# Kernel optimization log

Hardware: AMD Instinct MI355X
Metric: run time of the kernel (lower is better)

Reference implementation:

```python
import jax, jax.numpy as jnp
import numpy as np

E, H, KV, D = 2048, 32, 8, 64  # embed_dim, n_head, n_kv_head, head_dim
B, C = 1, 2048
G = H // KV  # GQA group size = 4


def setup_inputs() -> dict:
    key = jax.random.key(0)
    k0, k1, k2, k3, k4 = jax.random.split(key, 5)
    s = 0.02
    return {
        "x": jax.random.normal(k0, (B, C, E), dtype=jnp.float32),
        "W_q": jax.random.normal(k1, (H * D, E), dtype=jnp.float32) * s,
        "W_k": jax.random.normal(k2, (KV * D, E), dtype=jnp.float32) * s,
        "W_v": jax.random.normal(k3, (KV * D, E), dtype=jnp.float32) * s,
        "W_o": jax.random.normal(k4, (E, H * D), dtype=jnp.float32) * s,
    }


def reference(x, W_q, W_k, W_v, W_o):
    b, c, e = x.shape
    # bias-free projections (nn.Linear applies x @ W.T)
    Q = (x @ W_q.T).reshape(b, c, KV, G, D)   # [B,C,KV,G,D]
    K = (x @ W_k.T).reshape(b, c, KV, D)      # [B,C,KV,D]
    V = (x @ W_v.T).reshape(b, c, KV, D)
    scale = 1.0 / jnp.sqrt(jnp.float32(D))
    # grouped-query attention scores: query heads grouped per KV head
    scores = jnp.einsum("bqkgd,bskd->bkgqs", Q, K) * scale  # [B,KV,G,Cq,Cs]
    causal = jnp.tril(jnp.ones((c, c), dtype=bool))
    scores = jnp.where(causal, scores, jnp.finfo(scores.dtype).min)
    attn = jax.nn.softmax(scores, axis=-1)
    hidden = jnp.einsum("bkgqs,bskd->bqkgd", attn, V)  # [B,Cq,KV,G,D]
    hidden = hidden.reshape(b, c, H * D)
    return hidden @ W_o.T
```

## Files before the change

kernel.cpp:

```cpp
#include <hip/hip_runtime.h>
#include <stdint.h>
#include <stddef.h>

#define CLEN 2048
#define EMB  2048
#define NH   32
#define NKV  8
#define HD   64

#define SZ_X  (CLEN * EMB)
#define SZ_WQ (NH * HD * EMB)
#define SZ_WK (NKV * HD * EMB)
#define SZ_WV (NKV * HD * EMB)
#define SZ_WO (EMB * NH * HD)
#define SZ_ALL (SZ_X + SZ_WQ + SZ_WK + SZ_WV + SZ_WO)

typedef __attribute__((ext_vector_type(8))) short short8v;
typedef __attribute__((ext_vector_type(4))) short short4v;
typedef __attribute__((ext_vector_type(4))) float float4v;

#define MFMA16(A, B, C) __builtin_amdgcn_mfma_f32_16x16x32_bf16((A), (B), (C), 0, 0, 0)

#define SCL 0.1803368801111244f

__device__ __forceinline__ uint16_t f2bf(float f) {
  union { float f; unsigned int u; } c;
  c.f = f;
  return (uint16_t)((c.u + 0x7fffu + ((c.u >> 16) & 1u)) >> 16);
}
__device__ __forceinline__ uint16_t f2bf_c(float f) {
  union { float f; unsigned int u; } c;
  c.f = f;
  return (uint16_t)((c.u + 0x8000u) >> 16);
}

__device__ __forceinline__ void gload_lds16(const uint16_t* g, uint16_t* l) {
  __builtin_amdgcn_global_load_lds((const __attribute__((address_space(1))) void*)g,
                                   (__attribute__((address_space(3))) void*)l, 16, 0, 0);
}

__global__ __launch_bounds__(256) void cvt_all(
    const float* __restrict__ s0, const float* __restrict__ s1,
    const float* __restrict__ s2, const float* __restrict__ s3,
    const float* __restrict__ s4, uint16_t* __restrict__ dst)
{
  const long i = ((long)blockIdx.x * 256 + threadIdx.x) * 4;
  if (i >= SZ_ALL) return;
  const float* src;
  long off;
  if (i < SZ_X)                         { src = s0; off = i; }
  else if (i < SZ_X + SZ_WQ)            { src = s1; off = i - SZ_X; }
  else if (i < SZ_X + SZ_WQ + SZ_WK)    { src = s2; off = i - (SZ_X + SZ_WQ); }
  else if (i < SZ_X + SZ_WQ + SZ_WK + SZ_WV) { src = s3; off = i - (SZ_X + SZ_WQ + SZ_WK); }
  else                                  { src = s4; off = i - (SZ_X + SZ_WQ + SZ_WK + SZ_WV); }
  const float4v v = *(const float4v*)(src + off);
  short4v p;
#pragma unroll
  for (int j = 0; j < 4; ++j) p[j] = (short)f2bf(v[j]);
  *(short4v*)(dst + i) = p;
}

template <int NW, int OMODE>
__device__ __forceinline__ void gemm_bk64(
    const uint16_t* __restrict__ A, const uint16_t* __restrict__ B,
    uint16_t* __restrict__ Co, float* __restrict__ Cf,
    int m0, int n0, int M, int N, int Kd, float oscale)
{
  __shared__ uint16_t As[128 * 64];
  __shared__ uint16_t Bs[32 * NW * 64];
  const int tid = threadIdx.x;
  const int w = tid >> 6, l = tid & 63;
  const int wr = (w >> 1) << 5;
  const int wc = (w & 1) * (NW << 4);
  const int lr = l & 15, lhi = l >> 4;
  const int swz = (lr & 7) << 4;

  float4v acc[2][NW] = {};

  const int sr8 = l >> 3;
  const int scol = (((l & 7) ^ sr8) << 3);

  for (int k0 = 0; k0 < Kd; k0 += 64) {
    __syncthreads();
    gload_lds16(A + (size_t)(m0 + (w << 3) + sr8) * Kd + k0 + scol,       As + w * 512);
    gload_lds16(A + (size_t)(m0 + ((w + 8) << 3) + sr8) * Kd + k0 + scol, As + (w + 8) * 512);
    gload_lds16(B + (size_t)(n0 + (w << 3) + sr8) * Kd + k0 + scol,       Bs + w * 512);
    if (NW == 4)
      gload_lds16(B + (size_t)(n0 + ((w + 8) << 3) + sr8) * Kd + k0 + scol, Bs + (w + 8) * 512);
    __syncthreads();

    short8v a[2][2], b[NW][2];
#pragma unroll
    for (int i = 0; i < 2; ++i) {
      const int row = wr + i * 16 + lr;
#pragma unroll
      for (int ks = 0; ks < 2; ++ks)
        a[i][ks] = *(const short8v*)((const char*)As + row * 128 + ((ks * 64 + lhi * 16) ^ swz));
    }
#pragma unroll
    for (int j = 0; j < NW; ++j) {
      const int row = wc + j * 16 + lr;
#pragma unroll
      for (int ks = 0; ks < 2; ++ks)
        b[j][ks] = *(const short8v*)((const char*)Bs + row * 128 + ((ks * 64 + lhi * 16) ^ swz));
    }
#pragma unroll
    for (int ks = 0; ks < 2; ++ks)
#pragma unroll
      for (int i = 0; i < 2; ++i)
#pragma unroll
        for (int j = 0; j < NW; ++j)
          acc[i][j] = MFMA16(a[i][ks], b[j][ks], acc[i][j]);
  }

  if (OMODE == 1) {
#pragma unroll
    for (int i = 0; i < 2; ++i) {
      const int m = m0 + wr + i * 16 + lhi * 4;
#pragma unroll
      for (int j = 0; j < NW; ++j) {
        const int n = n0 + wc + j * 16 + lr;
        short4v pk;
#pragma unroll
        for (int r = 0; r < 4; ++r) pk[r] = (short)f2bf(acc[i][j][r]);
        *(short4v*)(Co + (size_t)n * M + m) = pk;
      }
    }
  } else if (OMODE == 0) {
#pragma unroll
    for (int i = 0; i < 2; ++i) {
      const int m = m0 + wr + i * 16 + lhi * 4;
#pragma unroll
      for (int j = 0; j < NW; ++j) {
        const int n = n0 + wc + j * 16 + lr;
#pragma unroll
        for (int r = 0; r < 4; ++r)
          Co[(size_t)(m + r) * N + n] = f2bf(acc[i][j][r] * oscale);
      }
    }
  } else {
#pragma unroll
    for (int i = 0; i < 2; ++i) {
      const int m = m0 + wr + i * 16 + lhi * 4;
#pragma unroll
      for (int j = 0; j < NW; ++j) {
        const int n = n0 + wc + j * 16 + lr;
#pragma unroll
        for (int r = 0; r < 4; ++r)
          Cf[(size_t)(m + r) * N + n] = acc[i][j][r];
      }
    }
  }
}

__global__ __launch_bounds__(512) void qkv_gemm(
    const uint16_t* __restrict__ x,
    const uint16_t* __restrict__ Wq, const uint16_t* __restrict__ Wk,
    const uint16_t* __restrict__ Wv,
    uint16_t* __restrict__ Qw, uint16_t* __restrict__ Kw, uint16_t* __restrict__ Vtw)
{
  const int m0 = blockIdx.x << 7;
  const int bn = blockIdx.y;
  if (bn < 16) {
    gemm_bk64<4, 0>(x, Wq, Qw, nullptr, m0, bn << 7, CLEN, NH * HD, EMB, SCL);
  } else if (bn < 24) {
    gemm_bk64<2, 0>(x, Wk, Kw, nullptr, m0, (bn - 16) << 6, CLEN, NKV * HD, EMB, 1.0f);
  } else {
    gemm_bk64<2, 1>(x, Wv, Vtw, nullptr, m0, (bn - 24) << 6, CLEN, NKV * HD, EMB, 1.0f);
  }
}

__global__ __launch_bounds__(512) void out_gemm(
    const uint16_t* __restrict__ Hh, const uint16_t* __restrict__ Wo,
    float* __restrict__ out)
{
  gemm_bk64<2, 2>(Hh, Wo, nullptr, out, blockIdx.x << 7, blockIdx.y << 6, CLEN, EMB, NH * HD, 1.0f);
}

__global__ __launch_bounds__(512) void attn_fwd(
    const uint16_t* __restrict__ Q, const uint16_t* __restrict__ Kx,
    const uint16_t* __restrict__ Vt, uint16_t* __restrict__ Hd)
{
  const int kvh = blockIdx.y;
  const int xp = blockIdx.x;
  const int tid = threadIdx.x, w = tid >> 6, l = tid & 63;
  const int lr = l & 15, lhi = l >> 4;
  const int h = (kvh << 2) | (w >> 1);
  const int wq = (w & 1) << 4;

  __shared__ uint16_t Ks[2][64 * 64];
  __shared__ uint16_t Vs[2][64 * 64];
  __shared__ uint16_t Pl[8][16 * 72];

  short8v ones;
#pragma unroll
  for (int c = 0; c < 8; ++c) ones[c] = (short)0x3F80;

  const int sr8 = l >> 3;
  const int scol = (((l & 7) ^ sr8) << 3);
  const int srow = (w << 3) | sr8;

  for (int it = 0; it < 2; ++it) {
    const int x = it ? (63 - xp) : xp;
    const int q0 = x << 5;
    const int qoff = (x & 1) << 5;
    const int ntile = (x >> 1) + 1;

    short8v qf0, qf1;
    {
      const uint16_t* qp = Q + (size_t)(q0 + wq + lr) * (NH * HD) + h * HD + lhi * 8;
      qf0 = *(const short8v*)qp;
      qf1 = *(const short8v*)(qp + 32);
    }

    float4v o[4] = {};
    float4v osum = {};

    gload_lds16(Kx + (size_t)srow * (NKV * HD) + kvh * HD + scol, Ks[0] + w * 512);
    gload_lds16(Vt + (size_t)(kvh * HD + srow) * CLEN + scol,     Vs[0] + w * 512);
    __syncthreads();

    int cur = 0;
    for (int s = 0; s < ntile; ++s) {
      if (s + 1 < ntile) {
        const int kv1 = (s + 1) << 6;
        gload_lds16(Kx + (size_t)(kv1 + srow) * (NKV * HD) + kvh * HD + scol,
                    Ks[cur ^ 1] + w * 512);
        gload_lds16(Vt + (size_t)(kvh * HD + srow) * CLEN + kv1 + scol,
                    Vs[cur ^ 1] + w * 512);
      }

      const char* KsB = (const char*)Ks[cur];
      const char* VsB = (const char*)Vs[cur];

      float4v sf[4];
      __builtin_amdgcn_s_setprio(1);
#pragma unroll
      for (int nb = 0; nb < 4; ++nb) {
        const int row = nb * 16 + lr;
        const int rowb = row * 128, sw = (row & 7) << 4;
        float4v a0 = {};
        a0 = MFMA16(qf0, *(const short8v*)(KsB + ((rowb + lhi * 16) ^ sw)), a0);
        a0 = MFMA16(qf1, *(const short8v*)(KsB + ((rowb + 64 + lhi * 16) ^ sw)), a0);
        sf[nb] = a0;
      }
      __builtin_amdgcn_s_setprio(0);

      if (s == ntile - 1) {
        const int qb = qoff + wq + lhi * 4;
#pragma unroll
        for (int nb = 0; nb < 4; ++nb)
#pragma unroll
          for (int r = 0; r < 4; ++r) {
            const float vv = (nb * 16 + lr <= qb + r) ? sf[nb][r] : -3e38f;
            sf[nb][r] = __builtin_amdgcn_exp2f(vv);
          }
      } else {
#pragma unroll
        for (int nb = 0; nb < 4; ++nb)
#pragma unroll
          for (int r = 0; r < 4; ++r)
            sf[nb][r] = __builtin_amdgcn_exp2f(sf[nb][r]);
      }

#pragma unroll
      for (int nb = 0; nb < 4; ++nb)
#pragma unroll
        for (int r = 0; r < 4; ++r)
          Pl[w][(lhi * 4 + r) * 72 + nb * 16 + lr] = f2bf_c(sf[nb][r]);
      const short8v pf0 = *(const short8v*)&Pl[w][lr * 72 + lhi * 8];
      const short8v pf1 = *(const short8v*)&Pl[w][lr * 72 + 32 + lhi * 8];

      __builtin_amdgcn_s_setprio(1);
#pragma unroll
      for (int j = 0; j < 4; ++j) {
        const int row = j * 16 + lr;
        const int rowb = row * 128, sw = (row & 7) << 4;
        o[j] = MFMA16(pf0, *(const short8v*)(VsB + ((rowb + lhi * 16) ^ sw)), o[j]);
        o[j] = MFMA16(pf1, *(const short8v*)(VsB + ((rowb + 64 + lhi * 16) ^ sw)), o[j]);
      }
      osum = MFMA16(pf0, ones, osum);
      osum = MFMA16(pf1, ones, osum);
      __builtin_amdgcn_s_setprio(0);

      __syncthreads();
      cur ^= 1;
    }

#pragma unroll
    for (int r = 0; r < 4; ++r) {
      const float inv = 1.0f / osum[r];
      const size_t qq = (size_t)(q0 + wq + lhi * 4 + r);
#pragma unroll
      for (int j = 0; j < 4; ++j)
        Hd[qq * (NH * HD) + h * HD + j * 16 + lr] = f2bf(o[j][r] * inv);
    }
  }
}

extern "C" void kernel_launch(void* const* d_in, const int* in_sizes, int n_in,
                              void* d_out, int out_size, void* d_ws, size_t ws_size,
                              hipStream_t stream) {
  const float* x  = (const float*)d_in[0];
  const float* Wq = (const float*)d_in[1];
  const float* Wk = (const float*)d_in[2];
  const float* Wv = (const float*)d_in[3];
  const float* Wo = (const float*)d_in[4];

  uint16_t* ws  = (uint16_t*)d_ws;
  uint16_t* xb  = ws;
  uint16_t* Wqb = xb  + SZ_X;
  uint16_t* Wkb = Wqb + SZ_WQ;
  uint16_t* Wvb = Wkb + SZ_WK;
  uint16_t* Wob = Wvb + SZ_WV;
  uint16_t* Qw  = Wob + SZ_WO;
  uint16_t* Kw  = Qw  + (size_t)CLEN * (NH * HD);
  uint16_t* Vtw = Kw  + (size_t)CLEN * (NKV * HD);
  uint16_t* Hw  = Vtw + (size_t)CLEN * (NKV * HD);

  cvt_all<<<SZ_ALL / 1024, 256, 0, stream>>>(x, Wq, Wk, Wv, Wo, ws);
  qkv_gemm<<<dim3(16, 32), 512, 0, stream>>>(xb, Wqb, Wkb, Wvb, Qw, Kw, Vtw);
  attn_fwd<<<dim3(32, 8), 512, 0, stream>>>(Qw, Kw, Vtw, Hw);
  out_gemm<<<dim3(16, 32), 512, 0, stream>>>(Hw, Wob, (float*)d_out);
}
```

Before: 114.9 us.

## Software-pipeline attention loop: overlap PV of previous tile with QK of current

```diff
diff --git a/kernel.cpp b/kernel.cpp
--- a/kernel.cpp
+++ b/kernel.cpp
@@ -189,7 +189,7 @@
   const int wq = (w & 1) << 4;
 
   __shared__ uint16_t Ks[2][64 * 64];
-  __shared__ uint16_t Vs[2][64 * 64];
+  __shared__ uint16_t Vs[3][64 * 64];
   __shared__ uint16_t Pl[8][16 * 72];
 
   short8v ones;
@@ -215,76 +215,87 @@
 
     float4v o[4] = {};
     float4v osum = {};
+    short8v pfP0 = {}, pfP1 = {};
 
     gload_lds16(Kx + (size_t)srow * (NKV * HD) + kvh * HD + scol, Ks[0] + w * 512);
     gload_lds16(Vt + (size_t)(kvh * HD + srow) * CLEN + scol,     Vs[0] + w * 512);
     __syncthreads();
 
-    int cur = 0;
-    for (int s = 0; s < ntile; ++s) {
-      if (s + 1 < ntile) {
-        const int kv1 = (s + 1) << 6;
+    int vw = 1;
+    int vr = 0;
+
+    for (int i = 0; i <= ntile; ++i) {
+      if (i + 1 < ntile) {
+        const int kv1 = (i + 1) << 6;
         gload_lds16(Kx + (size_t)(kv1 + srow) * (NKV * HD) + kvh * HD + scol,
-                    Ks[cur ^ 1] + w * 512);
+                    Ks[(i + 1) & 1] + w * 512);
         gload_lds16(Vt + (size_t)(kvh * HD + srow) * CLEN + kv1 + scol,
-                    Vs[cur ^ 1] + w * 512);
-      }
-
-      const char* KsB = (const char*)Ks[cur];
-      const char* VsB = (const char*)Vs[cur];
-
-      float4v sf[4];
-      __builtin_amdgcn_s_setprio(1);
-#pragma unroll
-      for (int nb = 0; nb < 4; ++nb) {
-        const int row = nb * 16 + lr;
-        const int rowb = row * 128, sw = (row & 7) << 4;
-        float4v a0 = {};
-        a0 = MFMA16(qf0, *(const short8v*)(KsB + ((rowb + lhi * 16) ^ sw)), a0);
-        a0 = MFMA16(qf1, *(const short8v*)(KsB + ((rowb + 64 + lhi * 16) ^ sw)), a0);
-        sf[nb] = a0;
-      }
-      __builtin_amdgcn_s_setprio(0);
-
-      if (s == ntile - 1) {
-        const int qb = qoff + wq + lhi * 4;
+                    Vs[vw] + w * 512);
+        vw = (vw == 2) ? 0 : vw + 1;
+      }
+
+      short8v pfC0, pfC1;
+      bool haveC = (i < ntile);
+      if (haveC) {
+        const char* KsB = (const char*)Ks[i & 1];
+        float4v sf[4];
+        __builtin_amdgcn_s_setprio(1);
+#pragma unroll
+        for (int nb = 0; nb < 4; ++nb) {
+          const int row = nb * 16 + lr;
+          const int rowb = row * 128, sw = (row & 7) << 4;
+          float4v a0 = {};
+          a0 = MFMA16(qf0, *(const short8v*)(KsB + ((rowb + lhi * 16) ^ sw)), a0);
+          a0 = MFMA16(qf1, *(const short8v*)(KsB + ((rowb + 64 + lhi * 16) ^ sw)), a0);
+          sf[nb] = a0;
+        }
+        __builtin_amdgcn_s_setprio(0);
+
+        if (i == ntile - 1) {
+          const int qb = qoff + wq + lhi * 4;
+#pragma unroll
+          for (int nb = 0; nb < 4; ++nb)
+#pragma unroll
+            for (int r = 0; r < 4; ++r) {
+              const float vv = (nb * 16 + lr <= qb + r) ? sf[nb][r] : -3e38f;
+              sf[nb][r] = __builtin_amdgcn_exp2f(vv);
+            }
+        } else {
+#pragma unroll
+          for (int nb = 0; nb < 4; ++nb)
+#pragma unroll
+            for (int r = 0; r < 4; ++r)
+              sf[nb][r] = __builtin_amdgcn_exp2f(sf[nb][r]);
+        }
+
 #pragma unroll
         for (int nb = 0; nb < 4; ++nb)
 #pragma unroll
-          for (int r = 0; r < 4; ++r) {
-            const float vv = (nb * 16 + lr <= qb + r) ? sf[nb][r] : -3e38f;
-            sf[nb][r] = __builtin_amdgcn_exp2f(vv);
-          }
-      } else {
-#pragma unroll
-        for (int nb = 0; nb < 4; ++nb)
-#pragma unroll
           for (int r = 0; r < 4; ++r)
-            sf[nb][r] = __builtin_amdgcn_exp2f(sf[nb][r]);
-      }
-
-#pragma unroll
-      for (int nb = 0; nb < 4; ++nb)
-#pragma unroll
-        for (int r = 0; r < 4; ++r)
-          Pl[w][(lhi * 4 + r) * 72 + nb * 16 + lr] = f2bf_c(sf[nb][r]);
-      const short8v pf0 = *(const short8v*)&Pl[w][lr * 72 + lhi * 8];
-      const short8v pf1 = *(const short8v*)&Pl[w][lr * 72 + 32 + lhi * 8];
-
-      __builtin_amdgcn_s_setprio(1);
-#pragma unroll
-      for (int j = 0; j < 4; ++j) {
-        const int row = j * 16 + lr;
-        const int rowb = row * 128, sw = (row & 7) << 4;
-        o[j] = MFMA16(pf0, *(const short8v*)(VsB + ((rowb + lhi * 16) ^ sw)), o[j]);
-        o[j] = MFMA16(pf1, *(const short8v*)(VsB + ((rowb + 64 + lhi * 16) ^ sw)), o[j]);
-      }
-      osum = MFMA16(pf0, ones, osum);
-      osum = MFMA16(pf1, ones, osum);
-      __builtin_amdgcn_s_setprio(0);
+            Pl[w][(lhi * 4 + r) * 72 + nb * 16 + lr] = f2bf_c(sf[nb][r]);
+        pfC0 = *(const short8v*)&Pl[w][lr * 72 + lhi * 8];
+        pfC1 = *(const short8v*)&Pl[w][lr * 72 + 32 + lhi * 8];
+      }
+
+      if (i >= 1) {
+        const char* VsB = (const char*)Vs[vr];
+        vr = (vr == 2) ? 0 : vr + 1;
+        __builtin_amdgcn_s_setprio(1);
+#pragma unroll
+        for (int j = 0; j < 4; ++j) {
+          const int row = j * 16 + lr;
+          const int rowb = row * 128, sw = (row & 7) << 4;
+          o[j] = MFMA16(pfP0, *(const short8v*)(VsB + ((rowb + lhi * 16) ^ sw)), o[j]);
+          o[j] = MFMA16(pfP1, *(const short8v*)(VsB + ((rowb + 64 + lhi * 16) ^ sw)), o[j]);
+        }
+        osum = MFMA16(pfP0, ones, osum);
+        osum = MFMA16(pfP1, ones, osum);
+        __builtin_amdgcn_s_setprio(0);
+      }
+
+      if (haveC) { pfP0 = pfC0; pfP1 = pfC1; }
 
       __syncthreads();
-      cur ^= 1;
     }
 
 #pragma unroll
```

After: 121.1 us. 1.05x slower.

## Halve attention block to 4 waves, each covering 32 query rows

Applied to the files above, without the earlier changes.

```diff
diff --git a/kernel.cpp b/kernel.cpp
--- a/kernel.cpp
+++ b/kernel.cpp
@@ -177,7 +177,7 @@
   gemm_bk64<2, 2>(Hh, Wo, nullptr, out, blockIdx.x << 7, blockIdx.y << 6, CLEN, EMB, NH * HD, 1.0f);
 }
 
-__global__ __launch_bounds__(512) void attn_fwd(
+__global__ __launch_bounds__(256) void attn_fwd(
     const uint16_t* __restrict__ Q, const uint16_t* __restrict__ Kx,
     const uint16_t* __restrict__ Vt, uint16_t* __restrict__ Hd)
 {
@@ -185,12 +185,12 @@
   const int xp = blockIdx.x;
   const int tid = threadIdx.x, w = tid >> 6, l = tid & 63;
   const int lr = l & 15, lhi = l >> 4;
-  const int h = (kvh << 2) | (w >> 1);
-  const int wq = (w & 1) << 4;
+  const int h = (kvh << 2) | w;
+  const int swz = (lr & 7) << 4;
 
   __shared__ uint16_t Ks[2][64 * 64];
   __shared__ uint16_t Vs[2][64 * 64];
-  __shared__ uint16_t Pl[8][16 * 72];
+  __shared__ uint16_t Pl[4][32 * 72];
 
   short8v ones;
 #pragma unroll
@@ -198,7 +198,6 @@
 
   const int sr8 = l >> 3;
   const int scol = (((l & 7) ^ sr8) << 3);
-  const int srow = (w << 3) | sr8;
 
   for (int it = 0; it < 2; ++it) {
     const int x = it ? (63 - xp) : xp;
@@ -206,81 +205,122 @@
     const int qoff = (x & 1) << 5;
     const int ntile = (x >> 1) + 1;
 
-    short8v qf0, qf1;
-    {
-      const uint16_t* qp = Q + (size_t)(q0 + wq + lr) * (NH * HD) + h * HD + lhi * 8;
-      qf0 = *(const short8v*)qp;
-      qf1 = *(const short8v*)(qp + 32);
-    }
-
-    float4v o[4] = {};
-    float4v osum = {};
-
-    gload_lds16(Kx + (size_t)srow * (NKV * HD) + kvh * HD + scol, Ks[0] + w * 512);
-    gload_lds16(Vt + (size_t)(kvh * HD + srow) * CLEN + scol,     Vs[0] + w * 512);
+    short8v qf[2][2];
+#pragma unroll
+    for (int i = 0; i < 2; ++i) {
+      const uint16_t* qp = Q + (size_t)(q0 + i * 16 + lr) * (NH * HD) + h * HD + lhi * 8;
+      qf[i][0] = *(const short8v*)qp;
+      qf[i][1] = *(const short8v*)(qp + 32);
+    }
+
+    float4v o[2][4] = {};
+    float4v osum[2] = {};
+
+#pragma unroll
+    for (int ci = 0; ci < 2; ++ci) {
+      const int c = (ci << 2) | w;
+      const int srow = (c << 3) | sr8;
+      gload_lds16(Kx + (size_t)srow * (NKV * HD) + kvh * HD + scol, Ks[0] + c * 512);
+      gload_lds16(Vt + (size_t)(kvh * HD + srow) * CLEN + scol,     Vs[0] + c * 512);
+    }
     __syncthreads();
 
     int cur = 0;
     for (int s = 0; s < ntile; ++s) {
       if (s + 1 < ntile) {
         const int kv1 = (s + 1) << 6;
-        gload_lds16(Kx + (size_t)(kv1 + srow) * (NKV * HD) + kvh * HD + scol,
-                    Ks[cur ^ 1] + w * 512);
-        gload_lds16(Vt + (size_t)(kvh * HD + srow) * CLEN + kv1 + scol,
-                    Vs[cur ^ 1] + w * 512);
+#pragma unroll
+        for (int ci = 0; ci < 2; ++ci) {
+          const int c = (ci << 2) | w;
+          const int srow = (c << 3) | sr8;
+          gload_lds16(Kx + (size_t)(kv1 + srow) * (NKV * HD) + kvh * HD + scol,
+                      Ks[cur ^ 1] + c * 512);
+          gload_lds16(Vt + (size_t)(kvh * HD + srow) * CLEN + kv1 + scol,
+                      Vs[cur ^ 1] + c * 512);
+        }
       }
 
       const char* KsB = (const char*)Ks[cur];
       const char* VsB = (const char*)Vs[cur];
 
-      float4v sf[4];
+      short8v kb[4][2];
+#pragma unroll
+      for (int nb = 0; nb < 4; ++nb) {
+        const int rowb = (nb * 16 + lr) * 128;
+#pragma unroll
+        for (int ks = 0; ks < 2; ++ks)
+          kb[nb][ks] = *(const short8v*)(KsB + ((rowb) + ((ks * 64 + lhi * 16) ^ swz)));
+      }
+
+      float4v sf[2][4];
       __builtin_amdgcn_s_setprio(1);
 #pragma unroll
-      for (int nb = 0; nb < 4; ++nb) {
-        const int row = nb * 16 + lr;
-        const int rowb = row * 128, sw = (row & 7) << 4;
-        float4v a0 = {};
-        a0 = MFMA16(qf0, *(const short8v*)(KsB + ((rowb + lhi * 16) ^ sw)), a0);
-        a0 = MFMA16(qf1, *(const short8v*)(KsB + ((rowb + 64 + lhi * 16) ^ sw)), a0);
-        sf[nb] = a0;
-      }
+      for (int i = 0; i < 2; ++i)
+#pragma unroll
+        for (int nb = 0; nb < 4; ++nb) {
+          float4v a0 = {};
+          a0 = MFMA16(qf[i][0], kb[nb][0], a0);
+          a0 = MFMA16(qf[i][1], kb[nb][1], a0);
+          sf[i][nb] = a0;
+        }
       __builtin_amdgcn_s_setprio(0);
 
       if (s == ntile - 1) {
-        const int qb = qoff + wq + lhi * 4;
+#pragma unroll
+        for (int i = 0; i < 2; ++i) {
+          const int qb = qoff + i * 16 + lhi * 4;
+#pragma unroll
+          for (int nb = 0; nb < 4; ++nb)
+#pragma unroll
+            for (int r = 0; r < 4; ++r) {
+              const float vv = (nb * 16 + lr <= qb + r) ? sf[i][nb][r] : -3e38f;
+              sf[i][nb][r] = __builtin_amdgcn_exp2f(vv);
+            }
+        }
+      } else {
+#pragma unroll
+        for (int i = 0; i < 2; ++i)
+#pragma unroll
+          for (int nb = 0; nb < 4; ++nb)
+#pragma unroll
+            for (int r = 0; r < 4; ++r)
+              sf[i][nb][r] = __builtin_amdgcn_exp2f(sf[i][nb][r]);
+      }
+
+#pragma unroll
+      for (int i = 0; i < 2; ++i)
 #pragma unroll
         for (int nb = 0; nb < 4; ++nb)
 #pragma unroll
-          for (int r = 0; r < 4; ++r) {
-            const float vv = (nb * 16 + lr <= qb + r) ? sf[nb][r] : -3e38f;
-            sf[nb][r] = __builtin_amdgcn_exp2f(vv);
-          }
-      } else {
-#pragma unroll
-        for (int nb = 0; nb < 4; ++nb)
-#pragma unroll
           for (int r = 0; r < 4; ++r)
-            sf[nb][r] = __builtin_amdgcn_exp2f(sf[nb][r]);
-      }
-
-#pragma unroll
-      for (int nb = 0; nb < 4; ++nb)
-#pragma unroll
-        for (int r = 0; r < 4; ++r)
-          Pl[w][(lhi * 4 + r) * 72 + nb * 16 + lr] = f2bf_c(sf[nb][r]);
-      const short8v pf0 = *(const short8v*)&Pl[w][lr * 72 + lhi * 8];
-      const short8v pf1 = *(const short8v*)&Pl[w][lr * 72 + 32 + lhi * 8];
+            Pl[w][(i * 16 + lhi * 4 + r) * 72 + nb * 16 + lr] = f2bf_c(sf[i][nb][r]);
+      short8v pf[2][2];
+#pragma unroll
+      for (int i = 0; i < 2; ++i)
+#pragma unroll
+        for (int ks = 0; ks < 2; ++ks)
+          pf[i][ks] = *(const short8v*)&Pl[w][(i * 16 + lr) * 72 + ks * 32 + lhi * 8];
+
+      short8v vb[4][2];
+#pragma unroll
+      for (int j = 0; j < 4; ++j) {
+        const int rowb = (j * 16 + lr) * 128;
+#pragma unroll
+        for (int ks = 0; ks < 2; ++ks)
+          vb[j][ks] = *(const short8v*)(VsB + ((rowb) + ((ks * 64 + lhi * 16) ^ swz)));
+      }
 
       __builtin_amdgcn_s_setprio(1);
 #pragma unroll
-      for (int j = 0; j < 4; ++j) {
-        const int row = j * 16 + lr;
-        const int rowb = row * 128, sw = (row & 7) << 4;
-        o[j] = MFMA16(pf0, *(const short8v*)(VsB + ((rowb + lhi * 16) ^ sw)), o[j]);
-        o[j] = MFMA16(pf1, *(const short8v*)(VsB + ((rowb + 64 + lhi * 16) ^ sw)), o[j]);
-      }
-      osum = MFMA16(pf0, ones, osum);
-      osum = MFMA16(pf1, ones, osum);
+      for (int i = 0; i < 2; ++i) {
+#pragma unroll
+        for (int j = 0; j < 4; ++j) {
+          o[i][j] = MFMA16(pf[i][0], vb[j][0], o[i][j]);
+          o[i][j] = MFMA16(pf[i][1], vb[j][1], o[i][j]);
+        }
+        osum[i] = MFMA16(pf[i][0], ones, osum[i]);
+        osum[i] = MFMA16(pf[i][1], ones, osum[i]);
+      }
       __builtin_amdgcn_s_setprio(0);
 
       __syncthreads();
@@ -288,13 +328,15 @@
     }
 
 #pragma unroll
-    for (int r = 0; r < 4; ++r) {
-      const float inv = 1.0f / osum[r];
-      const size_t qq = (size_t)(q0 + wq + lhi * 4 + r);
-#pragma unroll
-      for (int j = 0; j < 4; ++j)
-        Hd[qq * (NH * HD) + h * HD + j * 16 + lr] = f2bf(o[j][r] * inv);
-    }
+    for (int i = 0; i < 2; ++i)
+#pragma unroll
+      for (int r = 0; r < 4; ++r) {
+        const float inv = 1.0f / osum[i][r];
+        const size_t qq = (size_t)(q0 + i * 16 + lhi * 4 + r);
+#pragma unroll
+        for (int j = 0; j < 4; ++j)
+          Hd[qq * (NH * HD) + h * HD + j * 16 + lr] = f2bf(o[i][j][r] * inv);
+      }
   }
 }
 
@@ -320,6 +362,6 @@
 
   cvt_all<<<SZ_ALL / 1024, 256, 0, stream>>>(x, Wq, Wk, Wv, Wo, ws);
   qkv_gemm<<<dim3(16, 32), 512, 0, stream>>>(xb, Wqb, Wkb, Wvb, Qw, Kw, Vtw);
-  attn_fwd<<<dim3(32, 8), 512, 0, stream>>>(Qw, Kw, Vtw, Hw);
+  attn_fwd<<<dim3(32, 8), 256, 0, stream>>>(Qw, Kw, Vtw, Hw);
   out_gemm<<<dim3(16, 32), 512, 0, stream>>>(Hw, Wob, (float*)d_out);
 }
```

Result: slower. 121.5 us (+5.8%).
